# Performance work log

Hardware: AMD Instinct MI355X
Metric: run time of the kernel (lower is better)

The kernel has to match this reference:

```python
import jax, jax.numpy as jnp
import numpy as np

N = 100000        # nodes
E = 3200000       # edges (avg degree 32)
F_IN = 512        # input node features
HIDDEN = 16       # hardcoded in GCN.__init__
NUM_CLASSES = 40


def setup_inputs() -> dict:
    key = jax.random.key(0)
    k1, k2, k3, k4 = jax.random.split(key, 4)
    edge_index = jax.random.randint(k1, (2, E), 0, N, dtype=jnp.int32)
    x = jax.random.normal(k2, (N, F_IN), dtype=jnp.float32)
    # GCNConv weights (glorot-ish scale) and biases
    W1 = jax.random.normal(k3, (F_IN, HIDDEN), dtype=jnp.float32) * (1.0 / np.sqrt(F_IN))
    b1 = jnp.zeros((HIDDEN,), dtype=jnp.float32)
    W2 = jax.random.normal(k4, (HIDDEN, NUM_CLASSES), dtype=jnp.float32) * (1.0 / np.sqrt(HIDDEN))
    b2 = jnp.zeros((NUM_CLASSES,), dtype=jnp.float32)
    return {"edge_index": edge_index, "x": x, "W1": W1, "b1": b1, "W2": W2, "b2": b2}


def _gcn_conv(x, src, dst, W, b, n):
    # PyG GCNConv: linear transform, symmetric-normalized scatter-add aggregation
    h = x @ W                                             # [N, out]
    deg = jax.ops.segment_sum(jnp.ones_like(dst, dtype=h.dtype), dst, num_segments=n)
    dinv = jnp.where(deg > 0, jax.lax.rsqrt(deg), 0.0)    # deg^{-1/2}
    norm = dinv[src] * dinv[dst]                          # [E_total]
    out = jax.ops.segment_sum(h[src] * norm[:, None], dst, num_segments=n)
    return out + b


def reference(edge_index, x, W1, b1, W2, b2):
    n = x.shape[0]
    # GCNConv adds self-loops by default
    loop = jnp.arange(n, dtype=edge_index.dtype)
    src = jnp.concatenate([edge_index[0], loop])
    dst = jnp.concatenate([edge_index[1], loop])
    h = _gcn_conv(x, src, dst, W1, b1, n)
    h = jax.nn.relu(h)
    # F.dropout(training=self.training) -> identity in eval mode
    h = _gcn_conv(h, src, dst, W2, b2, n)
    return jax.nn.log_softmax(h, axis=1)[::20]
```

## Files before the change

kernel.cpp:

```cpp
#include <hip/hip_runtime.h>
#include <hip/hip_bf16.h>
#include <cstdint>
#include <math.h>

#define F_IN 512
#define HID  16
#define NCLS 40
#define OUT_STRIDE 20
#define TB   256
#define NBA  256
#define CAP  16384

typedef __attribute__((ext_vector_type(8))) short short8;
typedef __attribute__((ext_vector_type(4))) float f32x4;

__device__ inline unsigned short f2bf(float f) {
    unsigned u = __float_as_uint(f);
    u += 0x7fff + ((u >> 16) & 1);
    return (unsigned short)(u >> 16);
}
__device__ inline float bf2f(unsigned v) {
    return __uint_as_float(v << 16);
}

__global__ __launch_bounds__(256) void k_part(const int* __restrict__ src,
                                              const int* __restrict__ dst,
                                              int* __restrict__ gcnt,
                                              unsigned* __restrict__ bin,
                                              const float* __restrict__ W1,
                                              uint4* __restrict__ bfragg,
                                              int E, int NB, int chunk) {
    int t = threadIdx.x, blk = blockIdx.x;
    if (blk >= NBA) {
        int idx = (blk - NBA) * 256 + t;
        int kstep = idx >> 6, ln = idx & 63;
        int col = ln & 15, k0 = kstep * 32 + (ln >> 4) * 8;
        unsigned up[4];
#pragma unroll
        for (int i = 0; i < 4; i++) {
            float a = W1[(k0 + 2 * i) * HID + col];
            float b = W1[(k0 + 2 * i + 1) * HID + col];
            up[i] = (unsigned)f2bf(a) | ((unsigned)f2bf(b) << 16);
        }
        bfragg[idx] = make_uint4(up[0], up[1], up[2], up[3]);
        return;
    }
    __shared__ int h[512];
    __shared__ int pos[512];
    for (int b = t; b < NB; b += 256) h[b] = 0;
    __syncthreads();
    int e0 = blk * chunk, e1 = min(E, e0 + chunk);
    for (int e = e0 + t; e < e1; e += 256) {
        int d = dst[e];
        atomicAdd(&h[d >> 8], 1);
    }
    __syncthreads();
    for (int b = t; b < NB; b += 256) {
        int c = h[b];
        int rb = c ? atomicAdd(&gcnt[b], c) : 0;
        pos[b] = b * CAP + rb;
    }
    __syncthreads();
    for (int e = e0 + t; e < e1; e += 256) {
        int d = dst[e];
        int s = src[e];
        int p = atomicAdd(&pos[d >> 8], 1);
        bin[p] = ((unsigned)s << 8) | (unsigned)(d & (TB - 1));
    }
}

__global__ __launch_bounds__(256) void k_sortb(const unsigned* __restrict__ bin,
                                               const int* __restrict__ gcnt,
                                               int* __restrict__ csr,
                                               int2* __restrict__ rng,
                                               float* __restrict__ dinv, int N) {
    __shared__ int cnt[TB], incl[TB], pos[TB];
    int t = threadIdx.x, b = blockIdx.x;
    cnt[t] = 0;
    __syncthreads();
    int j0 = b * CAP, count = gcnt[b];
    for (int j = t; j < count; j += 256)
        atomicAdd(&cnt[bin[j0 + j] & (TB - 1)], 1);
    __syncthreads();
    incl[t] = cnt[t];
    __syncthreads();
    for (int off = 1; off < TB; off <<= 1) {
        int v = (t >= off) ? incl[t - off] : 0;
        __syncthreads();
        incl[t] += v;
        __syncthreads();
    }
    int ex = incl[t] - cnt[t];
    pos[t] = ex;
    int node = b * TB + t;
    if (node < N) {
        rng[node] = make_int2(j0 + ex, j0 + ex + cnt[t]);
        dinv[node] = rsqrtf((float)cnt[t] + 1.0f);
    }
    __syncthreads();
    for (int j = t; j < count; j += 256) {
        unsigned v = bin[j0 + j];
        int p = atomicAdd(&pos[v & (TB - 1)], 1);
        csr[j0 + p] = (int)(v >> 8);
    }
}

__global__ __launch_bounds__(64) void k_gemm1m(const float* __restrict__ x,
                                               const uint4* __restrict__ bfragg,
                                               const float* __restrict__ dinv,
                                               unsigned short* __restrict__ h1b, int n) {
    int lane = threadIdx.x;
    int rows0 = blockIdx.x * 64;
    int arow = lane & 15, kgrp = lane >> 4;

    const float* xr[4];
#pragma unroll
    for (int rt = 0; rt < 4; rt++) {
        int r = rows0 + rt * 16 + arow;
        if (r >= n) r = n - 1;
        xr[rt] = x + (size_t)r * F_IN + kgrp * 8;
    }

    f32x4 acc[4];
#pragma unroll
    for (int rt = 0; rt < 4; rt++) acc[rt] = (f32x4){0.f, 0.f, 0.f, 0.f};

#pragma unroll 4
    for (int kstep = 0; kstep < 16; kstep++) {
        uint4 braw = bfragg[kstep * 64 + lane];
        short8 b;
        *(uint4*)&b = braw;
#pragma unroll
        for (int rt = 0; rt < 4; rt++) {
            float4 lo = *(const float4*)(xr[rt] + kstep * 32);
            float4 hi = *(const float4*)(xr[rt] + kstep * 32 + 4);
            __hip_bfloat162 c0 = __float22bfloat162_rn(make_float2(lo.x, lo.y));
            __hip_bfloat162 c1 = __float22bfloat162_rn(make_float2(lo.z, lo.w));
            __hip_bfloat162 c2 = __float22bfloat162_rn(make_float2(hi.x, hi.y));
            __hip_bfloat162 c3 = __float22bfloat162_rn(make_float2(hi.z, hi.w));
            uint4 araw;
            __builtin_memcpy(&araw.x, &c0, 4);
            __builtin_memcpy(&araw.y, &c1, 4);
            __builtin_memcpy(&araw.z, &c2, 4);
            __builtin_memcpy(&araw.w, &c3, 4);
            short8 a;
            *(uint4*)&a = araw;
            acc[rt] = __builtin_amdgcn_mfma_f32_16x16x32_bf16(a, b, acc[rt], 0, 0, 0);
        }
    }

    int col = lane & 15, rbase = (lane >> 4) * 4;
#pragma unroll
    for (int rt = 0; rt < 4; rt++) {
#pragma unroll
        for (int r = 0; r < 4; r++) {
            int row = rows0 + rt * 16 + rbase + r;
            if (row < n)
                h1b[(size_t)row * HID + col] = f2bf(acc[rt][r] * dinv[row]);
        }
    }
}

__global__ __launch_bounds__(256) void k_agg(const uint2* __restrict__ h1u2,
                                             const int* __restrict__ csr,
                                             const int2* __restrict__ rng,
                                             const float* __restrict__ dinv,
                                             const float* __restrict__ b1,
                                             uint2* __restrict__ zu2, int n) {
    int lane = threadIdx.x & 63;
    int wave0 = (blockIdx.x * blockDim.x + threadIdx.x) >> 6;
    int nwaves = (gridDim.x * blockDim.x) >> 6;
    int c2 = lane & 3;
    int sub = lane >> 2;
    float bl0 = b1[4 * c2 + 0], bl1 = b1[4 * c2 + 1];
    float bl2 = b1[4 * c2 + 2], bl3 = b1[4 * c2 + 3];
    for (int node = wave0; node < n; node += nwaves) {
        int2 r = rng[node];
        int s0 = r.x, s1 = r.y;
        float s[4] = {0.f, 0.f, 0.f, 0.f};
        int j = s0 + sub;
        int nxt = (j < s1) ? csr[j] : 0;
        for (; j < s1; j += 16) {
            int cur = nxt;
            int jn = j + 16;
            if (jn < s1) nxt = csr[jn];
            uint2 u = h1u2[(size_t)cur * 4 + c2];
            s[0] += bf2f(u.x & 0xffff); s[1] += bf2f(u.x >> 16);
            s[2] += bf2f(u.y & 0xffff); s[3] += bf2f(u.y >> 16);
        }
#pragma unroll
        for (int m = 4; m < 64; m <<= 1) {
            s[0] += __shfl_xor(s[0], m); s[1] += __shfl_xor(s[1], m);
            s[2] += __shfl_xor(s[2], m); s[3] += __shfl_xor(s[3], m);
        }
        uint2 us = h1u2[(size_t)node * 4 + c2];
        s[0] += bf2f(us.x & 0xffff); s[1] += bf2f(us.x >> 16);
        s[2] += bf2f(us.y & 0xffff); s[3] += bf2f(us.y >> 16);
        float dv = dinv[node];
        float p0 = dv * s[0] + bl0;
        float p1 = dv * s[1] + bl1;
        float p2 = dv * s[2] + bl2;
        float p3 = dv * s[3] + bl3;
        if (lane < 4) {
            uint2 o;
            o.x = (unsigned)f2bf(fmaxf(p0, 0.f) * dv) | ((unsigned)f2bf(fmaxf(p1, 0.f) * dv) << 16);
            o.y = (unsigned)f2bf(fmaxf(p2, 0.f) * dv) | ((unsigned)f2bf(fmaxf(p3, 0.f) * dv) << 16);
            zu2[(size_t)node * 4 + c2] = o;
        }
    }
}

__global__ void k_out(const unsigned short* __restrict__ zb,
                      const int* __restrict__ csr, const int2* __restrict__ rng,
                      const float* __restrict__ dinv, const float* __restrict__ W2,
                      const float* __restrict__ b2, float* __restrict__ out, int nOut) {
    int lane = threadIdx.x & 63;
    int wv = (blockIdx.x * blockDim.x + threadIdx.x) >> 6;
    if (wv >= nOut) return;
    int node = wv * OUT_STRIDE;
    int c = lane & 15, sub = lane >> 4;
    int2 r = rng[node];
    int s0 = r.x, s1 = r.y;
    float sum = 0.f;
    for (int j = s0 + sub; j < s1; j += 4)
        sum += bf2f(zb[(size_t)csr[j] * HID + c]);
    sum += __shfl_xor(sum, 16);
    sum += __shfl_xor(sum, 32);
    sum += bf2f(zb[(size_t)node * HID + c]);
    float a = dinv[node] * sum;

    int jj = lane < NCLS ? lane : 0;
    float v = 0.f;
#pragma unroll
    for (int cc = 0; cc < 16; cc++) {
        float ac = __shfl(a, cc);
        v = fmaf(ac, W2[cc * NCLS + jj], v);
    }
    v += b2[jj];

    float vm = lane < NCLS ? v : -INFINITY;
    for (int off = 1; off < 64; off <<= 1) vm = fmaxf(vm, __shfl_xor(vm, off));
    float ex = lane < NCLS ? expf(v - vm) : 0.f;
    float se = ex;
    for (int off = 1; off < 64; off <<= 1) se += __shfl_xor(se, off);
    float ls = logf(se);
    if (lane < NCLS) out[(size_t)wv * NCLS + lane] = v - vm - ls;
}

extern "C" void kernel_launch(void* const* d_in, const int* in_sizes, int n_in,
                              void* d_out, int out_size, void* d_ws, size_t ws_size,
                              hipStream_t stream) {
    const int E = in_sizes[0] / 2;
    const int N = in_sizes[1] / F_IN;
    const int nOut = (N + OUT_STRIDE - 1) / OUT_STRIDE;
    const int NB = (N + TB - 1) / TB;
    const int chunk = (E + NBA - 1) / NBA;

    const int* src = (const int*)d_in[0];
    const int* dst = src + E;
    const float* x  = (const float*)d_in[1];
    const float* W1 = (const float*)d_in[2];
    const float* b1 = (const float*)d_in[3];
    const float* W2 = (const float*)d_in[4];
    const float* b2 = (const float*)d_in[5];
    float* out = (float*)d_out;

    uint8_t* w = (uint8_t*)d_ws;
    size_t off = 0;
    auto carve = [&](size_t bytes) {
        void* p = w + off;
        off += (bytes + 15) & ~(size_t)15;
        return p;
    };
    float*          dinv  = (float*)carve((size_t)N * 4);
    int*            gcnt  = (int*)carve((size_t)NB * 4);
    unsigned*       bin   = (unsigned*)carve((size_t)NB * CAP * 4);
    int*            csr   = (int*)carve((size_t)NB * CAP * 4);
    int2*           rng   = (int2*)carve((size_t)N * 8);
    unsigned short* h1b   = (unsigned short*)carve((size_t)N * HID * 2);
    unsigned short* zb    = (unsigned short*)carve((size_t)N * HID * 2);
    uint4*          bfragg= (uint4*)carve((size_t)16 * 64 * 16);
    (void)ws_size; (void)n_in; (void)out_size;

    hipMemsetAsync(gcnt, 0, (size_t)NB * 4, stream);
    k_part <<<NBA + 4, 256, 0, stream>>>(src, dst, gcnt, bin, W1, bfragg, E, NB, chunk);
    k_sortb<<<NB, TB, 0, stream>>>(bin, gcnt, csr, rng, dinv, N);
    k_gemm1m<<<(N + 63) / 64, 64, 0, stream>>>(x, bfragg, dinv, h1b, N);
    k_agg  <<<2048, 256, 0, stream>>>((const uint2*)h1b, csr, rng, dinv, b1, (uint2*)zb, N);
    k_out  <<<(nOut * 64 + 255) / 256, 256, 0, stream>>>(zb, csr, rng, dinv, W2, b2, out, nOut);
}
```

Before: 173.5 us.

## Vectorize edge partition loads, stage B fragments in LDS, add nontemporal loads

The edge partition kernel now reads src/dst as int4 vectors and unrolls the atomics four ways, with a scalar tail loop for leftovers. The GEMM kernel copies the B fragments into shared memory once per block and reads x with nontemporal loads. The aggregation kernel issues the self-row load before the neighbor loop and reads csr with nontemporal loads, as does the output kernel. The aim is fewer load instructions and less cache pollution from streamed data. The int4 casts assume each chunk start is 16-byte aligned, and the extra 16 KB of LDS in the GEMM may reduce how many blocks fit per CU.

Result: no change. 172.8 us (-0.4%).

```diff
diff --git a/kernel.cpp b/kernel.cpp
--- a/kernel.cpp
+++ b/kernel.cpp
@@ -50,10 +50,18 @@
     for (int b = t; b < NB; b += 256) h[b] = 0;
     __syncthreads();
     int e0 = blk * chunk, e1 = min(E, e0 + chunk);
-    for (int e = e0 + t; e < e1; e += 256) {
-        int d = dst[e];
-        atomicAdd(&h[d >> 8], 1);
-    }
+    int nvec = (e1 - e0) >> 2;
+    const int4* d4 = (const int4*)(dst + e0);
+    const int4* s4 = (const int4*)(src + e0);
+    for (int i = t; i < nvec; i += 256) {
+        int4 d = d4[i];
+        atomicAdd(&h[d.x >> 8], 1);
+        atomicAdd(&h[d.y >> 8], 1);
+        atomicAdd(&h[d.z >> 8], 1);
+        atomicAdd(&h[d.w >> 8], 1);
+    }
+    for (int e = e0 + nvec * 4 + t; e < e1; e += 256)
+        atomicAdd(&h[dst[e] >> 8], 1);
     __syncthreads();
     for (int b = t; b < NB; b += 256) {
         int c = h[b];
@@ -61,9 +69,17 @@
         pos[b] = b * CAP + rb;
     }
     __syncthreads();
-    for (int e = e0 + t; e < e1; e += 256) {
-        int d = dst[e];
-        int s = src[e];
+    for (int i = t; i < nvec; i += 256) {
+        int4 d = d4[i];
+        int4 s = s4[i];
+        int p;
+        p = atomicAdd(&pos[d.x >> 8], 1); bin[p] = ((unsigned)s.x << 8) | (unsigned)(d.x & (TB - 1));
+        p = atomicAdd(&pos[d.y >> 8], 1); bin[p] = ((unsigned)s.y << 8) | (unsigned)(d.y & (TB - 1));
+        p = atomicAdd(&pos[d.z >> 8], 1); bin[p] = ((unsigned)s.z << 8) | (unsigned)(d.z & (TB - 1));
+        p = atomicAdd(&pos[d.w >> 8], 1); bin[p] = ((unsigned)s.w << 8) | (unsigned)(d.w & (TB - 1));
+    }
+    for (int e = e0 + nvec * 4 + t; e < e1; e += 256) {
+        int d = dst[e], s = src[e];
         int p = atomicAdd(&pos[d >> 8], 1);
         bin[p] = ((unsigned)s << 8) | (unsigned)(d & (TB - 1));
     }
@@ -109,7 +125,11 @@
                                                const uint4* __restrict__ bfragg,
                                                const float* __restrict__ dinv,
                                                unsigned short* __restrict__ h1b, int n) {
+    __shared__ uint4 bl[16 * 64];
     int lane = threadIdx.x;
+    for (int i = lane; i < 16 * 64; i += 64) bl[i] = bfragg[i];
+    __syncthreads();
+
     int rows0 = blockIdx.x * 64;
     int arow = lane & 15, kgrp = lane >> 4;
 
@@ -127,17 +147,17 @@
 
 #pragma unroll 4
     for (int kstep = 0; kstep < 16; kstep++) {
-        uint4 braw = bfragg[kstep * 64 + lane];
+        uint4 braw = bl[kstep * 64 + lane];
         short8 b;
         *(uint4*)&b = braw;
 #pragma unroll
         for (int rt = 0; rt < 4; rt++) {
-            float4 lo = *(const float4*)(xr[rt] + kstep * 32);
-            float4 hi = *(const float4*)(xr[rt] + kstep * 32 + 4);
-            __hip_bfloat162 c0 = __float22bfloat162_rn(make_float2(lo.x, lo.y));
-            __hip_bfloat162 c1 = __float22bfloat162_rn(make_float2(lo.z, lo.w));
-            __hip_bfloat162 c2 = __float22bfloat162_rn(make_float2(hi.x, hi.y));
-            __hip_bfloat162 c3 = __float22bfloat162_rn(make_float2(hi.z, hi.w));
+            f32x4 lo = __builtin_nontemporal_load((const f32x4*)(xr[rt] + kstep * 32));
+            f32x4 hi = __builtin_nontemporal_load((const f32x4*)(xr[rt] + kstep * 32 + 4));
+            __hip_bfloat162 c0 = __float22bfloat162_rn(make_float2(lo[0], lo[1]));
+            __hip_bfloat162 c1 = __float22bfloat162_rn(make_float2(lo[2], lo[3]));
+            __hip_bfloat162 c2 = __float22bfloat162_rn(make_float2(hi[0], hi[1]));
+            __hip_bfloat162 c3 = __float22bfloat162_rn(make_float2(hi[2], hi[3]));
             uint4 araw;
             __builtin_memcpy(&araw.x, &c0, 4);
             __builtin_memcpy(&araw.y, &c1, 4);
@@ -177,13 +197,14 @@
     for (int node = wave0; node < n; node += nwaves) {
         int2 r = rng[node];
         int s0 = r.x, s1 = r.y;
+        uint2 us = h1u2[(size_t)node * 4 + c2];
         float s[4] = {0.f, 0.f, 0.f, 0.f};
         int j = s0 + sub;
-        int nxt = (j < s1) ? csr[j] : 0;
+        int nxt = (j < s1) ? __builtin_nontemporal_load(&csr[j]) : 0;
         for (; j < s1; j += 16) {
             int cur = nxt;
             int jn = j + 16;
-            if (jn < s1) nxt = csr[jn];
+            if (jn < s1) nxt = __builtin_nontemporal_load(&csr[jn]);
             uint2 u = h1u2[(size_t)cur * 4 + c2];
             s[0] += bf2f(u.x & 0xffff); s[1] += bf2f(u.x >> 16);
             s[2] += bf2f(u.y & 0xffff); s[3] += bf2f(u.y >> 16);
@@ -193,7 +214,6 @@
             s[0] += __shfl_xor(s[0], m); s[1] += __shfl_xor(s[1], m);
             s[2] += __shfl_xor(s[2], m); s[3] += __shfl_xor(s[3], m);
         }
-        uint2 us = h1u2[(size_t)node * 4 + c2];
         s[0] += bf2f(us.x & 0xffff); s[1] += bf2f(us.x >> 16);
         s[2] += bf2f(us.y & 0xffff); s[3] += bf2f(us.y >> 16);
         float dv = dinv[node];
@@ -223,7 +243,7 @@
     int s0 = r.x, s1 = r.y;
     float sum = 0.f;
     for (int j = s0 + sub; j < s1; j += 4)
-        sum += bf2f(zb[(size_t)csr[j] * HID + c]);
+        sum += bf2f(zb[(size_t)__builtin_nontemporal_load(&csr[j]) * HID + c]);
     sum += __shfl_xor(sum, 16);
     sum += __shfl_xor(sum, 32);
     sum += bf2f(zb[(size_t)node * HID + c]);
@@ -282,7 +302,7 @@
     uint4*          bfragg= (uint4*)carve((size_t)16 * 64 * 16);
     (void)ws_size; (void)n_in; (void)out_size;
 
-    hipMemsetAsync(gcnt, 0, (size_t)NB * 4, stream);
+    (void)hipMemsetAsync(gcnt, 0, (size_t)NB * 4, stream);
     k_part <<<NBA + 4, 256, 0, stream>>>(src, dst, gcnt, bin, W1, bfragg, E, NB, chunk);
     k_sortb<<<NB, TB, 0, stream>>>(bin, gcnt, csr, rng, dinv, N);
     k_gemm1m<<<(N + 63) / 64, 64, 0, stream>>>(x, bfragg, dinv, h1b, N);
```
